# Performance work log

Hardware: AMD Instinct MI355X
Metric: run time of the kernel (lower is better)

## Reference

```python
import jax, jax.numpy as jnp
import numpy as np

B, S, D, H = 4, 1024, 1024, 16
HD = D // H  # head dim 64
EPS = 1e-12

def setup_inputs() -> dict:
    key = jax.random.key(0)
    ks = jax.random.split(key, 10)
    sc = 1.0 / np.sqrt(D)
    return {
        "eeg": jax.random.normal(ks[0], (B, S, D), jnp.float32),
        "pic": jax.random.normal(ks[1], (B, S, D), jnp.float32),
        "Wk": jax.random.normal(ks[2], (D, D), jnp.float32) * sc,
        "bk": jnp.zeros((D,), jnp.float32),
        "Wq": jax.random.normal(ks[3], (D, D), jnp.float32) * sc,
        "bq": jnp.zeros((D,), jnp.float32),
        "Wv": jax.random.normal(ks[4], (D, D), jnp.float32) * sc,
        "bv": jnp.zeros((D,), jnp.float32),
        "Wd": jax.random.normal(ks[5], (D, D), jnp.float32) * sc,
        "bd": jnp.zeros((D,), jnp.float32),
        "ln_w": jnp.ones((D,), jnp.float32),
        "ln_b": jnp.zeros((D,), jnp.float32),
    }

def _heads(x):  # [B,S,D] -> [B,H,S,HD]
    return x.reshape(B, S, H, HD).transpose(0, 2, 1, 3)

def reference(eeg, pic, Wk, bk, Wq, bq, Wv, bv, Wd, bd, ln_w, ln_b):
    k = _heads(eeg @ Wk + bk)
    q = _heads(pic @ Wq + bq)
    v = _heads(pic @ Wv + bv)
    scores = jnp.einsum('bhqd,bhkd->bhqk', q, k) / jnp.sqrt(jnp.float32(HD))
    probs = jax.nn.softmax(scores, axis=-1)  # dropout = identity (eval mode)
    ctx = jnp.einsum('bhqk,bhkd->bhqd', probs, v)
    ctx = ctx.transpose(0, 2, 1, 3).reshape(B, S, D)
    h = ctx @ Wd + bd  # out_dropout = identity (eval)
    x = h + pic
    u = x.mean(-1, keepdims=True)
    s = ((x - u) ** 2).mean(-1, keepdims=True)
    x = (x - u) / jnp.sqrt(s + EPS)
    return ln_w * x + ln_b
```

## Files before the change

### kernel.cpp

```cpp
#include <hip/hip_runtime.h>
#include <hip/hip_bf16.h>

#define BB 4
#define SS 1024
#define DD 1024
#define HH 16
#define HD 64
#define MM (BB * SS)
#define LN_EPS 1e-12f

typedef unsigned short u16;
typedef __attribute__((ext_vector_type(8))) short bf16x8;
typedef __attribute__((ext_vector_type(4))) float f32x4;
typedef __attribute__((ext_vector_type(4))) unsigned short u16x4;
typedef __attribute__((ext_vector_type(8))) unsigned short u16x8;

__device__ __forceinline__ u16 f2bf(float f) {
    __hip_bfloat16 h = __float2bfloat16(f);
    u16 r; __builtin_memcpy(&r, &h, 2); return r;
}
__device__ __forceinline__ float bf2f(u16 u) {
    unsigned v = ((unsigned)u) << 16;
    float f; __builtin_memcpy(&f, &v, 4); return f;
}

typedef const __attribute__((address_space(1))) unsigned int* gas1_t;
typedef __attribute__((address_space(3))) unsigned int* las3_t;
__device__ __forceinline__ void gload16(const void* g, void* s) {
    __builtin_amdgcn_global_load_lds((gas1_t)g, (las3_t)s, 16, 0, 0);
}

__global__ __launch_bounds__(256) void conv2_bf16(
    const float* __restrict__ a, const float* __restrict__ c,
    u16* __restrict__ oa, u16* __restrict__ oc)
{
    const float* in = blockIdx.y ? c : a;
    u16* out = blockIdx.y ? oc : oa;
    size_t i = ((size_t)blockIdx.x * 256 + threadIdx.x) * 8;
    float4 x = *(const float4*)(in + i);
    float4 y = *(const float4*)(in + i + 4);
    u16x8 o;
    o[0]=f2bf(x.x); o[1]=f2bf(x.y); o[2]=f2bf(x.z); o[3]=f2bf(x.w);
    o[4]=f2bf(y.x); o[5]=f2bf(y.y); o[6]=f2bf(y.z); o[7]=f2bf(y.w);
    *(u16x8*)(out + i) = o;
}

__global__ __launch_bounds__(256) void transpose_w4(
    const float* __restrict__ W0, const float* __restrict__ W1,
    const float* __restrict__ W2, const float* __restrict__ W3,
    u16* __restrict__ T0, u16* __restrict__ T1,
    u16* __restrict__ T2, u16* __restrict__ T3)
{
    const int z = blockIdx.z;
    const float* W = (z==0)?W0:(z==1)?W1:(z==2)?W2:W3;
    u16* Wt = (z==0)?T0:(z==1)?T1:(z==2)?T2:T3;

    __shared__ float Ls[64][65];
    const int t = threadIdx.x;
    const int k0 = blockIdx.x * 64, n0 = blockIdx.y * 64;
    #pragma unroll
    for (int i = 0; i < 4; ++i) {
        int r = (t >> 4) + i * 16, c = (t & 15) * 4;
        float4 v = *(const float4*)&W[(size_t)(k0 + r) * DD + n0 + c];
        Ls[r][c] = v.x; Ls[r][c+1] = v.y; Ls[r][c+2] = v.z; Ls[r][c+3] = v.w;
    }
    __syncthreads();
    #pragma unroll
    for (int i = 0; i < 2; ++i) {
        int n = (t >> 3) + i * 32, kc = (t & 7) * 8;
        u16x8 o;
        #pragma unroll
        for (int j = 0; j < 8; ++j) o[j] = f2bf(Ls[kc + j][n]);
        *(u16x8*)&Wt[(size_t)(n0 + n) * DD + k0 + kc] = o;
    }
}

template<int TRANS>
__device__ __forceinline__ void gemm128_loop(
    const u16* __restrict__ A, const u16* __restrict__ Bt,
    int bm, int bn, u16* As, u16* Bs, f32x4 (&acc)[4][4])
{
    const int tid = threadIdx.x;
    const int w = tid >> 6, l = tid & 63, g = l >> 4, lr = l & 15;
    const int wm = w >> 1, wn = w & 1;

    const int srow = tid >> 3, ss = tid & 7;
    const int sgc = ss ^ (srow & 7);
    const u16* Ag = A + (size_t)(bm + srow) * DD + sgc * 8;
    const u16* Bg = Bt + (size_t)(bn + srow) * DD + sgc * 8;

    for (int k0 = 0; k0 < DD; k0 += 64) {
        #pragma unroll
        for (int rr = 0; rr < 4; ++rr)
            gload16(Ag + (size_t)rr * 32 * DD + k0, As + (rr * 256 + w * 64) * 8);
        #pragma unroll
        for (int rr = 0; rr < 4; ++rr)
            gload16(Bg + (size_t)rr * 32 * DD + k0, Bs + (rr * 256 + w * 64) * 8);
        __syncthreads();

        #pragma unroll
        for (int kh = 0; kh < 2; ++kh) {
            bf16x8 af[4], bfr[4];
            #pragma unroll
            for (int mi = 0; mi < 4; ++mi) {
                int row = wm * 64 + mi * 16 + lr;
                af[mi] = *(const bf16x8*)((const char*)As + row * 128 +
                                          ((kh * 4 + g) ^ (row & 7)) * 16);
            }
            #pragma unroll
            for (int ni = 0; ni < 4; ++ni) {
                int row = wn * 64 + ni * 16 + lr;
                bfr[ni] = *(const bf16x8*)((const char*)Bs + row * 128 +
                                           ((kh * 4 + g) ^ (row & 7)) * 16);
            }
            #pragma unroll
            for (int mi = 0; mi < 4; ++mi)
                #pragma unroll
                for (int ni = 0; ni < 4; ++ni) {
                    if (TRANS)
                        acc[ni][mi] = __builtin_amdgcn_mfma_f32_16x16x32_bf16(
                            bfr[ni], af[mi], acc[ni][mi], 0, 0, 0);
                    else
                        acc[mi][ni] = __builtin_amdgcn_mfma_f32_16x16x32_bf16(
                            af[mi], bfr[ni], acc[mi][ni], 0, 0, 0);
                }
        }
        __syncthreads();
    }
}

__global__ __launch_bounds__(256) void gemm_qkv(
    const u16* __restrict__ Ae, const u16* __restrict__ Ap,
    const u16* __restrict__ Bk, const u16* __restrict__ Bq, const u16* __restrict__ Bv,
    const float* __restrict__ bk, const float* __restrict__ bq, const float* __restrict__ bv,
    u16* __restrict__ Kb, u16* __restrict__ Qb, u16* __restrict__ VtG)
{
    const int i = (int)blockIdx.x;
    const int x = i & 7, j = i >> 3;
    const int sel = j >> 5;
    const int bn = ((j & 31) >> 2) * 128;
    const int bm = (x * 4 + (j & 3)) * 128;

    const u16* A  = sel ? Ap : Ae;
    const u16* Bt = (sel == 0) ? Bk : (sel == 1) ? Bq : Bv;
    const float* bias = (sel == 0) ? bk : (sel == 1) ? bq : bv;
    const float alpha = (sel == 1) ? 0.180336880111120f : 1.0f;

    __shared__ __align__(16) u16 As[128 * 64];
    __shared__ __align__(16) u16 Bs[128 * 64];

    f32x4 acc[4][4];
    #pragma unroll
    for (int a = 0; a < 4; ++a)
        #pragma unroll
        for (int b = 0; b < 4; ++b) { f32x4 z = {0,0,0,0}; acc[a][b] = z; }

    const int tid = threadIdx.x;
    const int w = tid >> 6, l = tid & 63, g = l >> 4, lr = l & 15;
    const int wm = w >> 1, wn = w & 1;

    if (sel == 2) {
        gemm128_loop<1>(A, Bt, bm, bn, As, Bs, acc);
        #pragma unroll
        for (int ni = 0; ni < 4; ++ni)
            #pragma unroll
            for (int r = 0; r < 4; ++r) {
                int n = bn + wn * 64 + ni * 16 + g * 4 + r;
                float bb = bias[n];
                #pragma unroll
                for (int mi = 0; mi < 4; ++mi) {
                    int m = bm + wm * 64 + mi * 16 + lr;
                    VtG[(size_t)n * MM + m] = f2bf(acc[ni][mi][r] + bb);
                }
            }
    } else {
        gemm128_loop<0>(A, Bt, bm, bn, As, Bs, acc);
        u16* C = sel ? Qb : Kb;
        float b4[4];
        #pragma unroll
        for (int ni = 0; ni < 4; ++ni) b4[ni] = bias[bn + wn * 64 + ni * 16 + lr];
        #pragma unroll
        for (int mi = 0; mi < 4; ++mi)
            #pragma unroll
            for (int ni = 0; ni < 4; ++ni)
                #pragma unroll
                for (int r = 0; r < 4; ++r) {
                    int row = bm + wm * 64 + mi * 16 + g * 4 + r;
                    int col = bn + wn * 64 + ni * 16 + lr;
                    C[(size_t)row * DD + col] = f2bf(alpha * (acc[mi][ni][r] + b4[ni]));
                }
    }
}

__global__ __launch_bounds__(256) void gemm_plain(
    const u16* __restrict__ A, const u16* __restrict__ Bt,
    const float* __restrict__ bias, u16* __restrict__ C)
{
    const int i = (int)blockIdx.x;
    const int x = i & 7, j = i >> 3;
    const int bn = (j >> 2) * 128;
    const int bm = (x * 4 + (j & 3)) * 128;

    __shared__ __align__(16) u16 As[128 * 64];
    __shared__ __align__(16) u16 Bs[128 * 64];

    f32x4 acc[4][4];
    #pragma unroll
    for (int a = 0; a < 4; ++a)
        #pragma unroll
        for (int b = 0; b < 4; ++b) { f32x4 z = {0,0,0,0}; acc[a][b] = z; }

    gemm128_loop<0>(A, Bt, bm, bn, As, Bs, acc);

    const int tid = threadIdx.x;
    const int w = tid >> 6, l = tid & 63, g = l >> 4, lr = l & 15;
    const int wm = w >> 1, wn = w & 1;
    float b4[4];
    #pragma unroll
    for (int ni = 0; ni < 4; ++ni) b4[ni] = bias[bn + wn * 64 + ni * 16 + lr];
    #pragma unroll
    for (int mi = 0; mi < 4; ++mi)
        #pragma unroll
        for (int ni = 0; ni < 4; ++ni)
            #pragma unroll
            for (int r = 0; r < 4; ++r) {
                int row = bm + wm * 64 + mi * 16 + g * 4 + r;
                int col = bn + wn * 64 + ni * 16 + lr;
                C[(size_t)row * DD + col] = f2bf(acc[mi][ni][r] + b4[ni]);
            }
}

__global__ __launch_bounds__(512) void attn_mfma(
    const u16* __restrict__ Q, const u16* __restrict__ K,
    const u16* __restrict__ Vt, u16* __restrict__ O)
{
    const int tid = threadIdx.x;
    const int w = tid >> 6, l = tid & 63, g = l >> 4, lr = l & 15;
    int bid = (int)blockIdx.x;
    bid = (bid & 7) * 64 + (bid >> 3);
    const int qb = bid & 7, h = (bid >> 3) & 15, b = bid >> 7;
    const size_t qrow0 = (size_t)b * SS + qb * 128;
    const size_t kv0 = (size_t)b * SS;
    const int hc = h * HD;

    __shared__ __align__(16) u16 Ks[2][64 * 64];
    __shared__ __align__(16) u16 Vs[2][64 * 64];
    __shared__ __align__(16) u16 Ps[8][16 * 72];

    const int srow = tid >> 3, ss = tid & 7;
    const int sgc = ss ^ (srow & 7);
    const u16* kg = K + (kv0 + srow) * DD + hc + sgc * 8;
    const u16* vg = Vt + (size_t)(hc + srow) * MM + kv0 + sgc * 8;

    bf16x8 qf[2];
    {
        const u16* qp = Q + (qrow0 + w * 16 + lr) * DD + hc + g * 8;
        qf[0] = *(const bf16x8*)(qp);
        qf[1] = *(const bf16x8*)(qp + 32);
    }

    f32x4 acc[4];
    #pragma unroll
    for (int dt = 0; dt < 4; ++dt) { f32x4 z = {0,0,0,0}; acc[dt] = z; }
    float m_run = -1e30f, l_run = 0.f;

    gload16(kg, &Ks[0][w * 512]);
    gload16(vg, &Vs[0][w * 512]);
    __syncthreads();

    for (int kb = 0; kb < SS / 64; ++kb) {
        const int cur = kb & 1;
        if (kb < SS / 64 - 1) {
            gload16(kg + (size_t)(kb + 1) * 64 * DD, &Ks[cur ^ 1][w * 512]);
            gload16(vg + (size_t)(kb + 1) * 64, &Vs[cur ^ 1][w * 512]);
        }
        const char* kbase = (const char*)&Ks[cur][0];
        const char* vbase = (const char*)&Vs[cur][0];

        f32x4 st[4];
        __builtin_amdgcn_s_setprio(1);
        #pragma unroll
        for (int kt = 0; kt < 4; ++kt) {
            int row = kt * 16 + lr;
            const char* rb = kbase + row * 128;
            bf16x8 k0 = *(const bf16x8*)(rb + ((0 + g) ^ (row & 7)) * 16);
            bf16x8 k1 = *(const bf16x8*)(rb + ((4 + g) ^ (row & 7)) * 16);
            f32x4 z = {0,0,0,0};
            z = __builtin_amdgcn_mfma_f32_16x16x32_bf16(k0, qf[0], z, 0, 0, 0);
            z = __builtin_amdgcn_mfma_f32_16x16x32_bf16(k1, qf[1], z, 0, 0, 0);
            st[kt] = z;
        }
        __builtin_amdgcn_s_setprio(0);

        float tmax = -1e30f;
        #pragma unroll
        for (int kt = 0; kt < 4; ++kt)
            #pragma unroll
            for (int r = 0; r < 4; ++r) tmax = fmaxf(tmax, st[kt][r]);
        tmax = fmaxf(tmax, __shfl_xor(tmax, 16));
        tmax = fmaxf(tmax, __shfl_xor(tmax, 32));

        if (!__all(tmax <= m_run + 8.f)) {
            float m_new = fmaxf(m_run, tmax);
            float sc = exp2f(m_run - m_new);
            m_run = m_new;
            l_run *= sc;
            float scq[4];
            #pragma unroll
            for (int r = 0; r < 4; ++r) scq[r] = __shfl(sc, g * 4 + r);
            #pragma unroll
            for (int dt = 0; dt < 4; ++dt)
                #pragma unroll
                for (int r = 0; r < 4; ++r) acc[dt][r] *= scq[r];
        }

        float p[16];
        float ps = 0.f;
        #pragma unroll
        for (int kt = 0; kt < 4; ++kt)
            #pragma unroll
            for (int r = 0; r < 4; ++r) {
                float v = exp2f(st[kt][r] - m_run);
                p[kt * 4 + r] = v;
                ps += v;
            }
        ps += __shfl_xor(ps, 16);
        ps += __shfl_xor(ps, 32);
        l_run += ps;

        #pragma unroll
        for (int kt = 0; kt < 4; ++kt) {
            u16x4 h4;
            #pragma unroll
            for (int r = 0; r < 4; ++r) h4[r] = f2bf(p[kt * 4 + r]);
            *(u16x4*)((char*)&Ps[w][0] + lr * 144 + kt * 32 + g * 8) = h4;
        }

        __builtin_amdgcn_s_setprio(1);
        #pragma unroll
        for (int kh = 0; kh < 2; ++kh) {
            bf16x8 pf = *(const bf16x8*)((const char*)&Ps[w][0] + lr * 144 +
                                         kh * 64 + g * 16);
            #pragma unroll
            for (int dt = 0; dt < 4; ++dt) {
                int row = dt * 16 + lr;
                bf16x8 vf = *(const bf16x8*)(vbase + row * 128 +
                                             ((kh * 4 + g) ^ (row & 7)) * 16);
                acc[dt] = __builtin_amdgcn_mfma_f32_16x16x32_bf16(pf, vf, acc[dt], 0, 0, 0);
            }
        }
        __builtin_amdgcn_s_setprio(0);

        __syncthreads();
    }

    float invl[4];
    #pragma unroll
    for (int r = 0; r < 4; ++r) invl[r] = 1.f / __shfl(l_run, g * 4 + r);
    #pragma unroll
    for (int dt = 0; dt < 4; ++dt)
        #pragma unroll
        for (int r = 0; r < 4; ++r) {
            size_t row = qrow0 + w * 16 + g * 4 + r;
            O[row * DD + hc + dt * 16 + lr] = f2bf(acc[dt][r] * invl[r]);
        }
}

__global__ __launch_bounds__(256) void ln_kernel(
    const u16* __restrict__ Hs, const float* __restrict__ P,
    const float* __restrict__ w, const float* __restrict__ bshift,
    float* __restrict__ out)
{
    const int row = blockIdx.x;
    const int tid = threadIdx.x;
    const size_t off = (size_t)row * DD;
    const int c0 = tid * 4;

    u16x4 h4 = *(const u16x4*)&Hs[off + c0];
    float4 p4 = *(const float4*)&P[off + c0];
    float x[4];
    x[0] = bf2f(h4[0]) + p4.x; x[1] = bf2f(h4[1]) + p4.y;
    x[2] = bf2f(h4[2]) + p4.z; x[3] = bf2f(h4[3]) + p4.w;

    float s = x[0] + x[1] + x[2] + x[3];
    #pragma unroll
    for (int o = 32; o >= 1; o >>= 1) s += __shfl_xor(s, o, 64);

    __shared__ float r1[4], r2[4];
    const int wid = tid >> 6;
    if ((tid & 63) == 0) r1[wid] = s;
    __syncthreads();
    const float mean = (r1[0] + r1[1] + r1[2] + r1[3]) * (1.f / (float)DD);

    float d2 = 0.f;
    #pragma unroll
    for (int i = 0; i < 4; ++i) { float d = x[i] - mean; d2 += d * d; }
    #pragma unroll
    for (int o = 32; o >= 1; o >>= 1) d2 += __shfl_xor(d2, o, 64);
    if ((tid & 63) == 0) r2[wid] = d2;
    __syncthreads();
    const float var = (r2[0] + r2[1] + r2[2] + r2[3]) * (1.f / (float)DD);
    const float inv = rsqrtf(var + LN_EPS);

    float4 o4;
    o4.x = w[c0 + 0] * ((x[0] - mean) * inv) + bshift[c0 + 0];
    o4.y = w[c0 + 1] * ((x[1] - mean) * inv) + bshift[c0 + 1];
    o4.z = w[c0 + 2] * ((x[2] - mean) * inv) + bshift[c0 + 2];
    o4.w = w[c0 + 3] * ((x[3] - mean) * inv) + bshift[c0 + 3];
    *(float4*)&out[off + c0] = o4;
}

extern "C" void kernel_launch(void* const* d_in, const int* in_sizes, int n_in,
                              void* d_out, int out_size, void* d_ws, size_t ws_size,
                              hipStream_t stream)
{
    const float* eeg = (const float*)d_in[0];
    const float* pic = (const float*)d_in[1];
    const float* Wk  = (const float*)d_in[2];
    const float* bk  = (const float*)d_in[3];
    const float* Wq  = (const float*)d_in[4];
    const float* bq  = (const float*)d_in[5];
    const float* Wv  = (const float*)d_in[6];
    const float* bv  = (const float*)d_in[7];
    const float* Wd  = (const float*)d_in[8];
    const float* bd  = (const float*)d_in[9];
    const float* lnw = (const float*)d_in[10];
    const float* lnb = (const float*)d_in[11];
    float* out = (float*)d_out;

    u16* ws = (u16*)d_ws;
    const size_t M4 = (size_t)1 << 22;
    u16* Ae  = ws;
    u16* Ap  = ws + M4;
    u16* WtK = ws + 2 * M4;
    u16* WtQ = WtK + (1u << 20);
    u16* WtV = WtQ + (1u << 20);
    u16* WtD = WtV + (1u << 20);
    u16* Kb  = ws + 3 * M4;
    u16* Qb  = ws + 4 * M4;
    u16* VtG = ws + 5 * M4;
    u16* Cb  = ws + 6 * M4;
    u16* Hb  = ws + 7 * M4;

    conv2_bf16<<<dim3(2048, 2), 256, 0, stream>>>(eeg, pic, Ae, Ap);
    transpose_w4<<<dim3(16, 16, 4), 256, 0, stream>>>(Wk, Wq, Wv, Wd,
                                                      WtK, WtQ, WtV, WtD);

    gemm_qkv<<<768, 256, 0, stream>>>(Ae, Ap, WtK, WtQ, WtV,
                                      bk, bq, bv, Kb, Qb, VtG);

    attn_mfma<<<BB * HH * (SS / 128), 512, 0, stream>>>(Qb, Kb, VtG, Cb);

    gemm_plain<<<256, 256, 0, stream>>>(Cb, WtD, bd, Hb);

    ln_kernel<<<MM, 256, 0, stream>>>(Hb, pic, lnw, lnb, out);
}
```

Before: 119.0 us.

## Rewrite QKV GEMM as 256x256 tile with phased double-buffered LDS pipeline

Measured after the change: 112.8 us. 5.2% less time.

```diff
diff --git a/kernel.cpp b/kernel.cpp
--- a/kernel.cpp
+++ b/kernel.cpp
@@ -28,6 +28,19 @@
 typedef __attribute__((address_space(3))) unsigned int* las3_t;
 __device__ __forceinline__ void gload16(const void* g, void* s) {
     __builtin_amdgcn_global_load_lds((gas1_t)g, (las3_t)s, 16, 0, 0);
+}
+
+__device__ __forceinline__ void vmw0() {
+    asm volatile("s_waitcnt vmcnt(0)" ::: "memory");
+    __builtin_amdgcn_sched_barrier(0);
+}
+__device__ __forceinline__ void vmw2() {
+    asm volatile("s_waitcnt vmcnt(2)" ::: "memory");
+    __builtin_amdgcn_sched_barrier(0);
+}
+__device__ __forceinline__ void vmw4() {
+    asm volatile("s_waitcnt vmcnt(4)" ::: "memory");
+    __builtin_amdgcn_sched_barrier(0);
 }
 
 __global__ __launch_bounds__(256) void conv2_bf16(
@@ -72,6 +85,150 @@
         #pragma unroll
         for (int j = 0; j < 8; ++j) o[j] = f2bf(Ls[kc + j][n]);
         *(u16x8*)&Wt[(size_t)(n0 + n) * DD + k0 + kc] = o;
+    }
+}
+
+template<int TRANS>
+__device__ __forceinline__ void do_phase(
+    const u16* Lcur, int wm, int wn, int g, int lr, int mh, int kh, f32x4* acc)
+{
+    const char* base = (const char*)Lcur;
+    bf16x8 af[4], bfr[4];
+    #pragma unroll
+    for (int i = 0; i < 4; ++i) {
+        int row = wm * 128 + mh * 64 + i * 16 + lr;
+        af[i] = *(const bf16x8*)(base + row * 128 + ((kh * 4 + g) ^ (row & 7)) * 16);
+    }
+    #pragma unroll
+    for (int i = 0; i < 4; ++i) {
+        int row = wn * 64 + i * 16 + lr;
+        bfr[i] = *(const bf16x8*)(base + 32768 + row * 128 + ((kh * 4 + g) ^ (row & 7)) * 16);
+    }
+    __builtin_amdgcn_s_setprio(1);
+    #pragma unroll
+    for (int i = 0; i < 4; ++i)
+        #pragma unroll
+        for (int j = 0; j < 4; ++j) {
+            int mi = mh * 4 + i;
+            if (TRANS)
+                acc[j * 8 + mi] = __builtin_amdgcn_mfma_f32_16x16x32_bf16(
+                    bfr[j], af[i], acc[j * 8 + mi], 0, 0, 0);
+            else
+                acc[mi * 4 + j] = __builtin_amdgcn_mfma_f32_16x16x32_bf16(
+                    af[i], bfr[j], acc[mi * 4 + j], 0, 0, 0);
+        }
+    __builtin_amdgcn_s_setprio(0);
+}
+
+template<int TRANS>
+__device__ __forceinline__ void gemm256_8ph(
+    const u16* __restrict__ A, const u16* __restrict__ Bt,
+    int bm, int bn, u16* Ls, f32x4* acc)
+{
+    const int tid = threadIdx.x;
+    const int w = tid >> 6, l = tid & 63, g = l >> 4, lr = l & 15;
+    const int wm = w >> 2, wn = w & 3;
+
+    const int srow = tid >> 3;
+    const int sgc = (tid & 7) ^ (srow & 7);
+    const u16* Ag = A + (size_t)(bm + srow) * DD + sgc * 8;
+    const u16* Bg = Bt + (size_t)(bn + srow) * DD + sgc * 8;
+
+#define STA(buf, r, k0) gload16(Ag + (size_t)(r) * 64 * DD + (k0), (buf) + (r) * 4096 + w * 512)
+#define STB(buf, r, k0) gload16(Bg + (size_t)(r) * 64 * DD + (k0), (buf) + 16384 + (r) * 4096 + w * 512)
+
+    STB(Ls, 0, 0); STB(Ls, 1, 0);
+    STB(Ls, 2, 0); STB(Ls, 3, 0);
+    STA(Ls, 0, 0); STA(Ls, 2, 0);
+    STA(Ls, 1, 0); STA(Ls, 3, 0);
+
+    #pragma unroll 2
+    for (int t = 0; t < 16; ++t) {
+        const int cur = t & 1;
+        const u16* cb = Ls + cur * 32768;
+        u16* nb = Ls + (cur ^ 1) * 32768;
+        const int nk = (t + 1) * 64;
+        const bool last = (t == 15);
+
+        vmw2();
+        __builtin_amdgcn_s_barrier();
+        if (!last) { STB(nb, 0, nk); STB(nb, 1, nk); }
+        do_phase<TRANS>(cb, wm, wn, g, lr, 0, 0, acc);
+
+        __builtin_amdgcn_s_barrier();
+        if (!last) { STB(nb, 2, nk); STB(nb, 3, nk); }
+        do_phase<TRANS>(cb, wm, wn, g, lr, 0, 1, acc);
+
+        if (last) vmw0(); else vmw4();
+        __builtin_amdgcn_s_barrier();
+        if (!last) { STA(nb, 0, nk); STA(nb, 2, nk); }
+        do_phase<TRANS>(cb, wm, wn, g, lr, 1, 0, acc);
+
+        __builtin_amdgcn_s_barrier();
+        if (!last) { STA(nb, 1, nk); STA(nb, 3, nk); }
+        do_phase<TRANS>(cb, wm, wn, g, lr, 1, 1, acc);
+    }
+#undef STA
+#undef STB
+}
+
+__global__ __launch_bounds__(512, 2) void gemm_qkv(
+    const u16* __restrict__ Ae, const u16* __restrict__ Ap,
+    const u16* __restrict__ Bk, const u16* __restrict__ Bq, const u16* __restrict__ Bv,
+    const float* __restrict__ bk, const float* __restrict__ bq, const float* __restrict__ bv,
+    u16* __restrict__ Kb, u16* __restrict__ Qb, u16* __restrict__ VtG)
+{
+    const int i = (int)blockIdx.x;
+    const int x = i & 7, j = i >> 3;
+    const int sel = j >> 3, inner = j & 7;
+    const int bm = (x * 2 + (inner & 1)) * 256;
+    const int bn = (inner >> 1) * 256;
+
+    const u16* A  = sel ? Ap : Ae;
+    const u16* Bt = (sel == 0) ? Bk : (sel == 1) ? Bq : Bv;
+    const float* bias = (sel == 0) ? bk : (sel == 1) ? bq : bv;
+    const float alpha = (sel == 1) ? 0.180336880111120f : 1.0f;
+
+    __shared__ __align__(16) u16 Ls[2 * 32768];
+
+    f32x4 acc[32];
+    #pragma unroll
+    for (int k = 0; k < 32; ++k) { f32x4 z = {0,0,0,0}; acc[k] = z; }
+
+    const int tid = threadIdx.x;
+    const int w = tid >> 6, l = tid & 63, g = l >> 4, lr = l & 15;
+    const int wm = w >> 2, wn = w & 3;
+
+    if (sel == 2) {
+        gemm256_8ph<1>(A, Bt, bm, bn, Ls, acc);
+        #pragma unroll
+        for (int ni = 0; ni < 4; ++ni)
+            #pragma unroll
+            for (int r = 0; r < 4; ++r) {
+                int n = bn + wn * 64 + ni * 16 + g * 4 + r;
+                float bb = bias[n];
+                #pragma unroll
+                for (int mi = 0; mi < 8; ++mi) {
+                    int m = bm + wm * 128 + mi * 16 + lr;
+                    VtG[(size_t)n * MM + m] = f2bf(acc[ni * 8 + mi][r] + bb);
+                }
+            }
+    } else {
+        gemm256_8ph<0>(A, Bt, bm, bn, Ls, acc);
+        u16* C = sel ? Qb : Kb;
+        float b4[4];
+        #pragma unroll
+        for (int ni = 0; ni < 4; ++ni) b4[ni] = bias[bn + wn * 64 + ni * 16 + lr];
+        #pragma unroll
+        for (int mi = 0; mi < 8; ++mi)
+            #pragma unroll
+            for (int ni = 0; ni < 4; ++ni)
+                #pragma unroll
+                for (int r = 0; r < 4; ++r) {
+                    int row = bm + wm * 128 + mi * 16 + g * 4 + r;
+                    int col = bn + wn * 64 + ni * 16 + lr;
+                    C[(size_t)row * DD + col] = f2bf(alpha * (acc[mi * 4 + ni][r] + b4[ni]));
+                }
     }
 }
 
@@ -126,69 +283,6 @@
                 }
         }
         __syncthreads();
-    }
-}
-
-__global__ __launch_bounds__(256) void gemm_qkv(
-    const u16* __restrict__ Ae, const u16* __restrict__ Ap,
-    const u16* __restrict__ Bk, const u16* __restrict__ Bq, const u16* __restrict__ Bv,
-    const float* __restrict__ bk, const float* __restrict__ bq, const float* __restrict__ bv,
-    u16* __restrict__ Kb, u16* __restrict__ Qb, u16* __restrict__ VtG)
-{
-    const int i = (int)blockIdx.x;
-    const int x = i & 7, j = i >> 3;
-    const int sel = j >> 5;
-    const int bn = ((j & 31) >> 2) * 128;
-    const int bm = (x * 4 + (j & 3)) * 128;
-
-    const u16* A  = sel ? Ap : Ae;
-    const u16* Bt = (sel == 0) ? Bk : (sel == 1) ? Bq : Bv;
-    const float* bias = (sel == 0) ? bk : (sel == 1) ? bq : bv;
-    const float alpha = (sel == 1) ? 0.180336880111120f : 1.0f;
-
-    __shared__ __align__(16) u16 As[128 * 64];
-    __shared__ __align__(16) u16 Bs[128 * 64];
-
-    f32x4 acc[4][4];
-    #pragma unroll
-    for (int a = 0; a < 4; ++a)
-        #pragma unroll
-        for (int b = 0; b < 4; ++b) { f32x4 z = {0,0,0,0}; acc[a][b] = z; }
-
-    const int tid = threadIdx.x;
-    const int w = tid >> 6, l = tid & 63, g = l >> 4, lr = l & 15;
-    const int wm = w >> 1, wn = w & 1;
-
-    if (sel == 2) {
-        gemm128_loop<1>(A, Bt, bm, bn, As, Bs, acc);
-        #pragma unroll
-        for (int ni = 0; ni < 4; ++ni)
-            #pragma unroll
-            for (int r = 0; r < 4; ++r) {
-                int n = bn + wn * 64 + ni * 16 + g * 4 + r;
-                float bb = bias[n];
-                #pragma unroll
-                for (int mi = 0; mi < 4; ++mi) {
-                    int m = bm + wm * 64 + mi * 16 + lr;
-                    VtG[(size_t)n * MM + m] = f2bf(acc[ni][mi][r] + bb);
-                }
-            }
-    } else {
-        gemm128_loop<0>(A, Bt, bm, bn, As, Bs, acc);
-        u16* C = sel ? Qb : Kb;
-        float b4[4];
-        #pragma unroll
-        for (int ni = 0; ni < 4; ++ni) b4[ni] = bias[bn + wn * 64 + ni * 16 + lr];
-        #pragma unroll
-        for (int mi = 0; mi < 4; ++mi)
-            #pragma unroll
-            for (int ni = 0; ni < 4; ++ni)
-                #pragma unroll
-                for (int r = 0; r < 4; ++r) {
-                    int row = bm + wm * 64 + mi * 16 + g * 4 + r;
-                    int col = bn + wn * 64 + ni * 16 + lr;
-                    C[(size_t)row * DD + col] = f2bf(alpha * (acc[mi][ni][r] + b4[ni]));
-                }
     }
 }
 
@@ -446,7 +540,7 @@
     transpose_w4<<<dim3(16, 16, 4), 256, 0, stream>>>(Wk, Wq, Wv, Wd,
                                                       WtK, WtQ, WtV, WtD);
 
-    gemm_qkv<<<768, 256, 0, stream>>>(Ae, Ap, WtK, WtQ, WtV,
+    gemm_qkv<<<192, 512, 0, stream>>>(Ae, Ap, WtK, WtQ, WtV,
                                       bk, bq, bv, Kb, Qb, VtG);
 
     attn_mfma<<<BB * HH * (SS / 128), 512, 0, stream>>>(Qb, Kb, VtG, Cb);
```
